# Performance work log

Measured on AMD Instinct MI355X. Metric: run time of the kernel, lower is better.

## Reference

```python
import jax, jax.numpy as jnp
import numpy as np
import math

EMBED_DIM = 512
NUM_HEADS = 8
HEAD_DIM = EMBED_DIM // NUM_HEADS


def setup_inputs() -> dict:
    key = jax.random.key(0)
    ks = jax.random.split(key, 11)
    s = 1.0 / math.sqrt(EMBED_DIM)
    x = jax.random.normal(ks[0], (8, EMBED_DIM, 32, 32), dtype=jnp.float32)
    Wq = jax.random.uniform(ks[1], (EMBED_DIM, EMBED_DIM), jnp.float32, -s, s)
    bq = jax.random.uniform(ks[2], (EMBED_DIM,), jnp.float32, -s, s)
    Wk = jax.random.uniform(ks[3], (EMBED_DIM, EMBED_DIM), jnp.float32, -s, s)
    bk = jax.random.uniform(ks[4], (EMBED_DIM,), jnp.float32, -s, s)
    Wv = jax.random.uniform(ks[5], (EMBED_DIM, EMBED_DIM), jnp.float32, -s, s)
    bv = jax.random.uniform(ks[6], (EMBED_DIM,), jnp.float32, -s, s)
    Wo = jax.random.uniform(ks[7], (EMBED_DIM, EMBED_DIM), jnp.float32, -s, s)
    bo = jax.random.uniform(ks[8], (EMBED_DIM,), jnp.float32, -s, s)
    gamma = jnp.ones((EMBED_DIM,), jnp.float32)
    beta = jnp.zeros((EMBED_DIM,), jnp.float32)
    return {"x": x, "Wq": Wq, "bq": bq, "Wk": Wk, "bk": bk, "Wv": Wv,
            "bv": bv, "Wo": Wo, "bo": bo, "gamma": gamma, "beta": beta}


def layer_norm(x, gamma, beta, eps=1e-5):
    mu = jnp.mean(x, axis=-1, keepdims=True)
    var = jnp.mean(jnp.square(x - mu), axis=-1, keepdims=True)
    return (x - mu) * jax.lax.rsqrt(var + eps) * gamma + beta


def reference(x, Wq, bq, Wk, bk, Wv, bv, Wo, bo, gamma, beta):
    B, C, H, W = x.shape
    S = H * W
    # [B, S, C]
    x_flat = x.reshape(B, C, S).transpose(0, 2, 1)
    residual = x_flat
    xn = layer_norm(x_flat, gamma, beta)
    # torch Linear: y = x @ W^T + b
    q = (xn @ Wq.T + bq).reshape(B, S, NUM_HEADS, HEAD_DIM)
    k = (xn @ Wk.T + bk).reshape(B, S, NUM_HEADS, HEAD_DIM)
    v = (xn @ Wv.T + bv).reshape(B, S, NUM_HEADS, HEAD_DIM)
    scale = 1.0 / math.sqrt(HEAD_DIM)
    scores = jnp.einsum('bqhd,bkhd->bhqk', q, k) * scale
    attn = jax.nn.softmax(scores, axis=-1)  # dropout is identity in eval
    out = jnp.einsum('bhqk,bkhd->bqhd', attn, v).reshape(B, S, C)
    out = out @ Wo.T + bo + residual
    return out.transpose(0, 2, 1).reshape(B, C, H, W)
```

## Files before the change

kernel.cpp:

```cpp
#include <hip/hip_runtime.h>
#include <hip/hip_bf16.h>

typedef __bf16 bf16_t;
typedef __bf16 bf16x8 __attribute__((ext_vector_type(8)));
typedef float floatx4 __attribute__((ext_vector_type(4)));

#define EMBED 512
#define S_LEN 1024
#define NH 8
#define HD 64
#define LDQ 1568

#define MFMA16(a, b, c) __builtin_amdgcn_mfma_f32_16x16x32_bf16(a, b, c, 0, 0, 0)

static __device__ __forceinline__ bf16_t f2bf(float f) {
    unsigned int x = __builtin_bit_cast(unsigned int, f);
    unsigned int lsb = (x >> 16) & 1u;
    x += 0x7fffu + lsb;
    unsigned short u = (unsigned short)(x >> 16);
    return __builtin_bit_cast(bf16_t, u);
}
static __device__ __forceinline__ float bf2f(bf16_t v) {
    unsigned short u = __builtin_bit_cast(unsigned short, v);
    unsigned int x = ((unsigned int)u) << 16;
    return __builtin_bit_cast(float, x);
}
static __device__ __forceinline__ unsigned int pack2(float lo, float hi) {
    return (__builtin_bit_cast(unsigned int, lo) >> 16) |
           (__builtin_bit_cast(unsigned int, hi) & 0xFFFF0000u);
}

__global__ __launch_bounds__(256) void cvt4_kernel(const float* __restrict__ s0,
                                                   const float* __restrict__ s1,
                                                   const float* __restrict__ s2,
                                                   const float* __restrict__ s3,
                                                   bf16_t* __restrict__ d0,
                                                   bf16_t* __restrict__ d1,
                                                   bf16_t* __restrict__ d2,
                                                   bf16_t* __restrict__ d3) {
    const float* s; bf16_t* d;
    switch (blockIdx.y) {
        case 0:  s = s0; d = d0; break;
        case 1:  s = s1; d = d1; break;
        case 2:  s = s2; d = d2; break;
        default: s = s3; d = d3; break;
    }
    int i = (blockIdx.x * 256 + threadIdx.x) * 8;
#pragma unroll
    for (int j = 0; j < 8; ++j) d[i + j] = f2bf(s[i + j]);
}

__global__ __launch_bounds__(256) void ln_stats_kernel(const float* __restrict__ x,
                                                       float* __restrict__ muA,
                                                       float* __restrict__ rsA) {
    int bid = blockIdx.x;
    int b = bid >> 5, s0 = (bid & 31) * 32;
    int t = threadIdx.x, tc = t >> 5, ts = t & 31;
    const float* xp = x + (size_t)b * EMBED * S_LEN + s0 + ts;
    float sm = 0.f, sq = 0.f;
    for (int i = 0; i < 64; ++i) {
        float v = xp[(size_t)(tc * 64 + i) * S_LEN];
        sm += v; sq += v * v;
    }
    __shared__ float Sm[8][32], Sq[8][32];
    Sm[tc][ts] = sm; Sq[tc][ts] = sq;
    __syncthreads();
    if (t < 32) {
        float m = 0.f, q = 0.f;
#pragma unroll
        for (int j = 0; j < 8; ++j) { m += Sm[j][t]; q += Sq[j][t]; }
        float mu = m * (1.0f / EMBED);
        float var = q * (1.0f / EMBED) - mu * mu;
        muA[b * S_LEN + s0 + t] = mu;
        rsA[b * S_LEN + s0 + t] = rsqrtf(var + 1e-5f);
    }
}

__global__ __launch_bounds__(256) void ln_tr_kernel(const float* __restrict__ x,
                                                    const float* __restrict__ muA,
                                                    const float* __restrict__ rsA,
                                                    const float* __restrict__ gamma,
                                                    const float* __restrict__ beta,
                                                    bf16_t* __restrict__ xn) {
    __shared__ float T[32][33];
    int tx = threadIdx.x & 31, ty = threadIdx.x >> 5;
    int b = blockIdx.z, c0 = blockIdx.y * 32, s0 = blockIdx.x * 32;
#pragma unroll
    for (int i = 0; i < 4; ++i) {
        int cr = ty + i * 8;
        T[cr][tx] = x[((size_t)b * EMBED + c0 + cr) * S_LEN + s0 + tx];
    }
    __syncthreads();
    float g = gamma[c0 + tx], be = beta[c0 + tx];
#pragma unroll
    for (int i = 0; i < 4; ++i) {
        int sr = ty + i * 8;
        float mu = muA[b * S_LEN + s0 + sr];
        float rs = rsA[b * S_LEN + s0 + sr];
        xn[((size_t)b * S_LEN + s0 + sr) * EMBED + c0 + tx] =
            f2bf((T[tx][sr] - mu) * rs * g + be);
    }
}

__global__ __launch_bounds__(256) void gemm_kernel(const bf16_t* __restrict__ X,
                                                   const bf16_t* __restrict__ W,
                                                   const float* __restrict__ b0,
                                                   const float* __restrict__ b1,
                                                   const float* __restrict__ b2,
                                                   bf16_t* __restrict__ Y, int ldY) {
    __shared__ __align__(16) bf16_t Wl[2][128 * 72];
    int t = threadIdx.x;
    int col0 = blockIdx.y * 128, row0 = blockIdx.x * 128;
    int scol = t >> 1, sseg = (t & 1) * 32;
    const bf16_t* wsrc = W + (size_t)(col0 + scol) * EMBED + sseg;
    {
        bf16x8 r0 = *(const bf16x8*)(wsrc);
        bf16x8 r1 = *(const bf16x8*)(wsrc + 8);
        bf16x8 r2 = *(const bf16x8*)(wsrc + 16);
        bf16x8 r3 = *(const bf16x8*)(wsrc + 24);
        bf16_t* d = &Wl[0][scol * 72 + sseg];
        *(bf16x8*)d = r0;        *(bf16x8*)(d + 8) = r1;
        *(bf16x8*)(d + 16) = r2; *(bf16x8*)(d + 24) = r3;
    }
    int lane = t & 63, w = t >> 6, g = lane >> 4, n16 = lane & 15;
    int rw0 = row0 + w * 32;
    const bf16_t* xr0 = X + (size_t)(rw0 + n16) * EMBED + g * 8;
    const bf16_t* xr1 = xr0 + (size_t)16 * EMBED;
    bf16x8 a00 = *(const bf16x8*)(xr0);
    bf16x8 a01 = *(const bf16x8*)(xr0 + 32);
    bf16x8 a10 = *(const bf16x8*)(xr1);
    bf16x8 a11 = *(const bf16x8*)(xr1 + 32);
    __syncthreads();
    floatx4 acc[2][8] = {};
#pragma unroll
    for (int kc = 0; kc < 8; ++kc) {
        bf16x8 p0, p1, p2, p3, na00, na01, na10, na11;
        if (kc < 7) {
            int ko = (kc + 1) * 64;
            p0 = *(const bf16x8*)(wsrc + ko);
            p1 = *(const bf16x8*)(wsrc + ko + 8);
            p2 = *(const bf16x8*)(wsrc + ko + 16);
            p3 = *(const bf16x8*)(wsrc + ko + 24);
            na00 = *(const bf16x8*)(xr0 + ko);
            na01 = *(const bf16x8*)(xr0 + ko + 32);
            na10 = *(const bf16x8*)(xr1 + ko);
            na11 = *(const bf16x8*)(xr1 + ko + 32);
        }
        const bf16_t* wl = &Wl[kc & 1][0];
#pragma unroll
        for (int kk = 0; kk < 2; ++kk) {
            bf16x8 s0 = (kk == 0) ? a00 : a01;
            bf16x8 s1 = (kk == 0) ? a10 : a11;
#pragma unroll
            for (int nt = 0; nt < 8; ++nt) {
                bf16x8 bfr = *(const bf16x8*)(&wl[(nt * 16 + n16) * 72 + kk * 32 + g * 8]);
                acc[0][nt] = MFMA16(s0, bfr, acc[0][nt]);
                acc[1][nt] = MFMA16(s1, bfr, acc[1][nt]);
            }
        }
        if (kc < 7) {
            bf16_t* d = &Wl[(kc + 1) & 1][scol * 72 + sseg];
            *(bf16x8*)d = p0;        *(bf16x8*)(d + 8) = p1;
            *(bf16x8*)(d + 16) = p2; *(bf16x8*)(d + 24) = p3;
            a00 = na00; a01 = na01; a10 = na10; a11 = na11;
        }
        __syncthreads();
    }
#pragma unroll
    for (int ar = 0; ar < 2; ++ar)
#pragma unroll
        for (int nt = 0; nt < 8; ++nt) {
            int col = col0 + nt * 16 + n16;
            float bv = (col < 512) ? b0[col]
                     : (col < 1024) ? b1[col - 512] : b2[col - 1024];
#pragma unroll
            for (int r = 0; r < 4; ++r) {
                int row = rw0 + ar * 16 + g * 4 + r;
                Y[(size_t)row * ldY + col] = f2bf(acc[ar][nt][r] + bv);
            }
        }
}

__global__ __launch_bounds__(256) void wsgemm_out_kernel(const bf16_t* __restrict__ Wb,
                                                         const bf16_t* __restrict__ act,
                                                         const float* __restrict__ bias,
                                                         const float* __restrict__ xres,
                                                         float* __restrict__ out) {
    __shared__ __align__(16) bf16_t Al[2][64 * 72];
    int b = blockIdx.z, n0 = blockIdx.x * 64, m0 = blockIdx.y * 128;
    int t = threadIdx.x;
    int srow = t >> 2, sseg = (t & 3) * 16;
    const bf16_t* asrc = act + ((size_t)b * S_LEN + n0 + srow) * EMBED + sseg;
    {
        bf16x8 r0 = *(const bf16x8*)(asrc);
        bf16x8 r1 = *(const bf16x8*)(asrc + 8);
        bf16_t* d = &Al[0][srow * 72 + sseg];
        *(bf16x8*)d = r0; *(bf16x8*)(d + 8) = r1;
    }
    int lane = t & 63, w = t >> 6, g = lane >> 4, n16 = lane & 15;
    int mw = m0 + w * 32;
    const bf16_t* wr0 = Wb + (size_t)(mw + n16) * EMBED + g * 8;
    const bf16_t* wr1 = wr0 + (size_t)16 * EMBED;
    bf16x8 a00 = *(const bf16x8*)(wr0);
    bf16x8 a01 = *(const bf16x8*)(wr0 + 32);
    bf16x8 a10 = *(const bf16x8*)(wr1);
    bf16x8 a11 = *(const bf16x8*)(wr1 + 32);
    __syncthreads();
    floatx4 acc[2][4] = {};
#pragma unroll
    for (int kc = 0; kc < 8; ++kc) {
        bf16x8 p0, p1, na00, na01, na10, na11;
        if (kc < 7) {
            int ko = (kc + 1) * 64;
            p0 = *(const bf16x8*)(asrc + ko);
            p1 = *(const bf16x8*)(asrc + ko + 8);
            na00 = *(const bf16x8*)(wr0 + ko);
            na01 = *(const bf16x8*)(wr0 + ko + 32);
            na10 = *(const bf16x8*)(wr1 + ko);
            na11 = *(const bf16x8*)(wr1 + ko + 32);
        }
        const bf16_t* al = &Al[kc & 1][0];
#pragma unroll
        for (int kk = 0; kk < 2; ++kk) {
            bf16x8 s0 = (kk == 0) ? a00 : a01;
            bf16x8 s1 = (kk == 0) ? a10 : a11;
#pragma unroll
            for (int nt = 0; nt < 4; ++nt) {
                bf16x8 bfr = *(const bf16x8*)(&al[(nt * 16 + n16) * 72 + kk * 32 + g * 8]);
                acc[0][nt] = MFMA16(s0, bfr, acc[0][nt]);
                acc[1][nt] = MFMA16(s1, bfr, acc[1][nt]);
            }
        }
        if (kc < 7) {
            bf16_t* d = &Al[(kc + 1) & 1][srow * 72 + sseg];
            *(bf16x8*)d = p0; *(bf16x8*)(d + 8) = p1;
            a00 = na00; a01 = na01; a10 = na10; a11 = na11;
        }
        __syncthreads();
    }
#pragma unroll
    for (int ar = 0; ar < 2; ++ar)
#pragma unroll
        for (int r = 0; r < 4; ++r) {
            int row = mw + ar * 16 + g * 4 + r;
            float bv = bias[row];
#pragma unroll
            for (int nt = 0; nt < 4; ++nt) {
                int col = n0 + nt * 16 + n16;
                size_t oi = ((size_t)b * EMBED + row) * S_LEN + col;
                out[oi] = acc[ar][nt][r] + bv + xres[oi];
            }
        }
}

__global__ __launch_bounds__(256) void attn_kernel(const bf16_t* __restrict__ qkv,
                                                   bf16_t* __restrict__ o) {
    __shared__ __align__(16) bf16_t Kt[2][64 * 72];
    __shared__ __align__(16) bf16_t Vt[2][64 * 72];
    __shared__ __align__(16) unsigned int Pl[4][2][16 * 36];
    int bid = blockIdx.x;
    int bh = bid & 63, qt = bid >> 6;
    int b = bh >> 3, h = bh & 7;
    int t = threadIdx.x, w = t >> 6, lane = t & 63, g = lane >> 4, n16 = lane & 15;
    size_t baseQ = (size_t)b * S_LEN * LDQ + h * HD;
    int qA = qt * 128 + w * 32 + n16;

    const bf16_t* qpA = qkv + baseQ + (size_t)qA * LDQ + g * 8;
    const bf16_t* qpB = qpA + (size_t)16 * LDQ;
    bf16x8 qa0 = *(const bf16x8*)(qpA);
    bf16x8 qa1 = *(const bf16x8*)(qpA + 32);
    bf16x8 qb0 = *(const bf16x8*)(qpB);
    bf16x8 qb1 = *(const bf16x8*)(qpB + 32);
#pragma unroll
    for (int j = 0; j < 8; ++j) {
        qa0[j] = f2bf(bf2f(qa0[j]) * 0.125f);
        qa1[j] = f2bf(bf2f(qa1[j]) * 0.125f);
        qb0[j] = f2bf(bf2f(qb0[j]) * 0.125f);
        qb1[j] = f2bf(bf2f(qb1[j]) * 0.125f);
    }

    int srow = t >> 2, scol = (t & 3) * 16;
    const bf16_t* ksrc = qkv + baseQ + 512 + (size_t)srow * LDQ + scol;
    const bf16_t* vsrc = qkv + baseQ + 1024 + (size_t)srow * LDQ + scol;
    {
        bf16x8 k0 = *(const bf16x8*)(ksrc);
        bf16x8 k1 = *(const bf16x8*)(ksrc + 8);
        bf16x8 v0 = *(const bf16x8*)(vsrc);
        bf16x8 v1 = *(const bf16x8*)(vsrc + 8);
        bf16_t* kd = &Kt[0][srow * 72 + scol];
        *(bf16x8*)kd = k0; *(bf16x8*)(kd + 8) = k1;
#pragma unroll
        for (int j = 0; j < 8; ++j) {
            Vt[0][(scol + j) * 72 + srow]     = v0[j];
            Vt[0][(scol + 8 + j) * 72 + srow] = v1[j];
        }
    }

    float lsA[4] = {}, lsB[4] = {};
    floatx4 oaccA[4] = {}, oaccB[4] = {};
    unsigned int* PLa = &Pl[w][0][0];
    unsigned int* PLb = &Pl[w][1][0];

    for (int it = 0; it < 16; ++it) {
        int cur = it & 1, nxt = cur ^ 1;
        __syncthreads();
        bf16x8 pk0, pk1, pv0, pv1;
        if (it < 15) {
            size_t adv = (size_t)(it + 1) * 64 * LDQ;
            pk0 = *(const bf16x8*)(ksrc + adv);
            pk1 = *(const bf16x8*)(ksrc + adv + 8);
            pv0 = *(const bf16x8*)(vsrc + adv);
            pv1 = *(const bf16x8*)(vsrc + adv + 8);
        }
        const bf16_t* Kl = &Kt[cur][0];
        const bf16_t* Vl = &Vt[cur][0];
        floatx4 sA[4], sB[4];
#pragma unroll
        for (int kb = 0; kb < 4; ++kb) {
            bf16x8 k0 = *(const bf16x8*)(&Kl[(kb * 16 + n16) * 72 + g * 8]);
            bf16x8 k1 = *(const bf16x8*)(&Kl[(kb * 16 + n16) * 72 + 32 + g * 8]);
            sA[kb] = floatx4{-12.f, -12.f, -12.f, -12.f};
            sA[kb] = MFMA16(k0, qa0, sA[kb]);
            sA[kb] = MFMA16(k1, qa1, sA[kb]);
            sB[kb] = floatx4{-12.f, -12.f, -12.f, -12.f};
            sB[kb] = MFMA16(k0, qb0, sB[kb]);
            sB[kb] = MFMA16(k1, qb1, sB[kb]);
        }
        if (it < 15) {
            bf16_t* kd = &Kt[nxt][srow * 72 + scol];
            *(bf16x8*)kd = pk0; *(bf16x8*)(kd + 8) = pk1;
#pragma unroll
            for (int j = 0; j < 8; ++j) {
                Vt[nxt][(scol + j) * 72 + srow]     = pv0[j];
                Vt[nxt][(scol + 8 + j) * 72 + srow] = pv1[j];
            }
        }
#pragma unroll
        for (int kb = 0; kb < 4; ++kb)
#pragma unroll
            for (int r = 0; r < 4; ++r) {
                float eA = __expf(fminf(sA[kb][r], 40.f));
                sA[kb][r] = eA; lsA[kb] += eA;
                float eB = __expf(fminf(sB[kb][r], 40.f));
                sB[kb][r] = eB; lsB[kb] += eB;
            }
#pragma unroll
        for (int kb = 0; kb < 4; ++kb) {
            uint2 prA, prB;
            prA.x = pack2(sA[kb][0], sA[kb][1]);
            prA.y = pack2(sA[kb][2], sA[kb][3]);
            *(uint2*)&PLa[n16 * 36 + kb * 8 + g * 2] = prA;
            prB.x = pack2(sB[kb][0], sB[kb][1]);
            prB.y = pack2(sB[kb][2], sB[kb][3]);
            *(uint2*)&PLb[n16 * 36 + kb * 8 + g * 2] = prB;
        }
        uint4 uA0 = *(const uint4*)&PLa[n16 * 36 + g * 4];
        uint4 uA1 = *(const uint4*)&PLa[n16 * 36 + 16 + g * 4];
        uint4 uB0 = *(const uint4*)&PLb[n16 * 36 + g * 4];
        uint4 uB1 = *(const uint4*)&PLb[n16 * 36 + 16 + g * 4];
        bf16x8 pfA0 = __builtin_bit_cast(bf16x8, uA0);
        bf16x8 pfA1 = __builtin_bit_cast(bf16x8, uA1);
        bf16x8 pfB0 = __builtin_bit_cast(bf16x8, uB0);
        bf16x8 pfB1 = __builtin_bit_cast(bf16x8, uB1);
#pragma unroll
        for (int dt = 0; dt < 4; ++dt) {
            bf16x8 v0 = *(const bf16x8*)(&Vl[(dt * 16 + n16) * 72 + g * 8]);
            bf16x8 v1 = *(const bf16x8*)(&Vl[(dt * 16 + n16) * 72 + 32 + g * 8]);
            oaccA[dt] = MFMA16(v0, pfA0, oaccA[dt]);
            oaccA[dt] = MFMA16(v1, pfA1, oaccA[dt]);
            oaccB[dt] = MFMA16(v0, pfB0, oaccB[dt]);
            oaccB[dt] = MFMA16(v1, pfB1, oaccB[dt]);
        }
    }
    float lA = (lsA[0] + lsA[1]) + (lsA[2] + lsA[3]);
    lA += __shfl_xor(lA, 16);
    lA += __shfl_xor(lA, 32);
    float lB = (lsB[0] + lsB[1]) + (lsB[2] + lsB[3]);
    lB += __shfl_xor(lB, 16);
    lB += __shfl_xor(lB, 32);
    float rlA = 1.0f / lA, rlB = 1.0f / lB;
    size_t orowA = ((size_t)b * S_LEN + qA) * EMBED + h * HD;
    size_t orowB = orowA + (size_t)16 * EMBED;
#pragma unroll
    for (int dt = 0; dt < 4; ++dt) {
        uint2 prA, prB;
        prA.x = pack2(oaccA[dt][0] * rlA, oaccA[dt][1] * rlA);
        prA.y = pack2(oaccA[dt][2] * rlA, oaccA[dt][3] * rlA);
        *(uint2*)(o + orowA + dt * 16 + g * 4) = prA;
        prB.x = pack2(oaccB[dt][0] * rlB, oaccB[dt][1] * rlB);
        prB.y = pack2(oaccB[dt][2] * rlB, oaccB[dt][3] * rlB);
        *(uint2*)(o + orowB + dt * 16 + g * 4) = prB;
    }
}

extern "C" void kernel_launch(void* const* d_in, const int* in_sizes, int n_in,
                              void* d_out, int out_size, void* d_ws, size_t ws_size,
                              hipStream_t stream) {
    const float* x     = (const float*)d_in[0];
    const float* Wq    = (const float*)d_in[1];
    const float* bq    = (const float*)d_in[2];
    const float* Wk    = (const float*)d_in[3];
    const float* bk    = (const float*)d_in[4];
    const float* Wv    = (const float*)d_in[5];
    const float* bv    = (const float*)d_in[6];
    const float* Wo    = (const float*)d_in[7];
    const float* bo    = (const float*)d_in[8];
    const float* gamma = (const float*)d_in[9];
    const float* beta  = (const float*)d_in[10];
    float* out = (float*)d_out;

    char* ws = (char*)d_ws;
    bf16_t* xn    = (bf16_t*)ws;
    bf16_t* qkvb  = (bf16_t*)(ws + 8388608);
    bf16_t* wqkv  = (bf16_t*)(ws + 34078720);
    bf16_t* wo    = (bf16_t*)(ws + 35651584);
    float*  muA   = (float*)(ws + 36175872);
    float*  rsA   = (float*)(ws + 36208640);
    bf16_t* ab    = xn;

    cvt4_kernel<<<dim3(128, 4), 256, 0, stream>>>(Wq, Wk, Wv, Wo,
                                                  wqkv, wqkv + 262144,
                                                  wqkv + 524288, wo);
    ln_stats_kernel<<<dim3(256), 256, 0, stream>>>(x, muA, rsA);
    ln_tr_kernel<<<dim3(32, 16, 8), 256, 0, stream>>>(x, muA, rsA, gamma, beta, xn);
    gemm_kernel<<<dim3(64, 12), 256, 0, stream>>>(xn, wqkv, bq, bk, bv, qkvb, LDQ);
    attn_kernel<<<dim3(512), 256, 0, stream>>>(qkvb, ab);
    wsgemm_out_kernel<<<dim3(16, 4, 8), 256, 0, stream>>>(wo, ab, bo, x, out);
}
```

Baseline: 180.1 us.

## Emit V transposed from QKV GEMM epilogue to drop per-tile LDS transpose in attention

The QKV projection now writes Q/K into a narrower row-major buffer and writes V in a per-channel (transposed) layout via an LDS-staged epilogue, storing it temporarily in the output buffer. The attention kernel then loads V tiles with vectorized contiguous reads and 16-byte LDS stores instead of 16 scalar scattered LDS writes per thread per tile. This targets LDS bank conflicts and scalar-store overhead in the attention inner loop, at the cost of an extra barrier and LDS round-trip in the GEMM epilogue and reuse of the output buffer as scratch.

```diff
diff --git a/kernel.cpp b/kernel.cpp
--- a/kernel.cpp
+++ b/kernel.cpp
@@ -9,7 +9,8 @@
 #define S_LEN 1024
 #define NH 8
 #define HD 64
-#define LDQ 1568
+#define LDK 1056
+#define LDV 1088
 
 #define MFMA16(a, b, c) __builtin_amdgcn_mfma_f32_16x16x32_bf16(a, b, c, 0, 0, 0)
 
@@ -28,6 +29,11 @@
 static __device__ __forceinline__ unsigned int pack2(float lo, float hi) {
     return (__builtin_bit_cast(unsigned int, lo) >> 16) |
            (__builtin_bit_cast(unsigned int, hi) & 0xFFFF0000u);
+}
+static __device__ __forceinline__ unsigned int pack2r(float lo, float hi) {
+    unsigned short a = __builtin_bit_cast(unsigned short, f2bf(lo));
+    unsigned short b = __builtin_bit_cast(unsigned short, f2bf(hi));
+    return (unsigned int)a | ((unsigned int)b << 16);
 }
 
 __global__ __launch_bounds__(256) void cvt4_kernel(const float* __restrict__ s0,
@@ -107,7 +113,8 @@
                                                    const float* __restrict__ b0,
                                                    const float* __restrict__ b1,
                                                    const float* __restrict__ b2,
-                                                   bf16_t* __restrict__ Y, int ldY) {
+                                                   bf16_t* __restrict__ Y,
+                                                   bf16_t* __restrict__ vtb) {
     __shared__ __align__(16) bf16_t Wl[2][128 * 72];
     int t = threadIdx.x;
     int col0 = blockIdx.y * 128, row0 = blockIdx.x * 128;
@@ -166,19 +173,42 @@
         }
         __syncthreads();
     }
-#pragma unroll
-    for (int ar = 0; ar < 2; ++ar)
-#pragma unroll
-        for (int nt = 0; nt < 8; ++nt) {
-            int col = col0 + nt * 16 + n16;
-            float bv = (col < 512) ? b0[col]
-                     : (col < 1024) ? b1[col - 512] : b2[col - 1024];
-#pragma unroll
-            for (int r = 0; r < 4; ++r) {
-                int row = rw0 + ar * 16 + g * 4 + r;
-                Y[(size_t)row * ldY + col] = f2bf(acc[ar][nt][r] + bv);
-            }
-        }
+    if (col0 < 1024) {
+        const float* bp = (col0 < 512) ? b0 : b1;
+#pragma unroll
+        for (int ar = 0; ar < 2; ++ar)
+#pragma unroll
+            for (int nt = 0; nt < 8; ++nt) {
+                int col = col0 + nt * 16 + n16;
+                float bv = bp[col & 511];
+#pragma unroll
+                for (int r = 0; r < 4; ++r) {
+                    int row = rw0 + ar * 16 + g * 4 + r;
+                    Y[(size_t)row * LDK + col] = f2bf(acc[ar][nt][r] + bv);
+                }
+            }
+    } else {
+        bf16_t* Tl = &Wl[0][0];
+#pragma unroll
+        for (int ar = 0; ar < 2; ++ar)
+#pragma unroll
+            for (int nt = 0; nt < 8; ++nt) {
+                int chl = nt * 16 + n16;
+                float bv = b2[(col0 & 511) + chl];
+                uint2 pr;
+                pr.x = pack2r(acc[ar][nt][0] + bv, acc[ar][nt][1] + bv);
+                pr.y = pack2r(acc[ar][nt][2] + bv, acc[ar][nt][3] + bv);
+                *(uint2*)(&Tl[chl * 136 + w * 32 + ar * 16 + g * 4]) = pr;
+            }
+        __syncthreads();
+        int ch = t >> 1, seg = (t & 1) * 64;
+        int bb = row0 >> 10, s0 = row0 & 1023;
+        bf16_t* dst = vtb + ((size_t)(bb * EMBED + (col0 - 1024) + ch)) * LDV + s0 + seg;
+        const bf16_t* srcl = &Tl[ch * 136 + seg];
+#pragma unroll
+        for (int i = 0; i < 8; ++i)
+            *(bf16x8*)(dst + i * 8) = *(const bf16x8*)(srcl + i * 8);
+    }
 }
 
 __global__ __launch_bounds__(256) void wsgemm_out_kernel(const bf16_t* __restrict__ Wb,
@@ -253,20 +283,22 @@
         }
 }
 
-__global__ __launch_bounds__(256) void attn_kernel(const bf16_t* __restrict__ qkv,
+__global__ __launch_bounds__(256) void attn_kernel(const bf16_t* __restrict__ qk,
+                                                   const bf16_t* __restrict__ vt,
                                                    bf16_t* __restrict__ o) {
     __shared__ __align__(16) bf16_t Kt[2][64 * 72];
-    __shared__ __align__(16) bf16_t Vt[2][64 * 72];
+    __shared__ __align__(16) bf16_t Vl2[2][64 * 72];
     __shared__ __align__(16) unsigned int Pl[4][2][16 * 36];
     int bid = blockIdx.x;
     int bh = bid & 63, qt = bid >> 6;
     int b = bh >> 3, h = bh & 7;
     int t = threadIdx.x, w = t >> 6, lane = t & 63, g = lane >> 4, n16 = lane & 15;
-    size_t baseQ = (size_t)b * S_LEN * LDQ + h * HD;
+    size_t baseQK = (size_t)b * S_LEN * LDK;
+    size_t baseV  = ((size_t)b * EMBED + h * HD) * LDV;
     int qA = qt * 128 + w * 32 + n16;
 
-    const bf16_t* qpA = qkv + baseQ + (size_t)qA * LDQ + g * 8;
-    const bf16_t* qpB = qpA + (size_t)16 * LDQ;
+    const bf16_t* qpA = qk + baseQK + (size_t)qA * LDK + h * HD + g * 8;
+    const bf16_t* qpB = qpA + (size_t)16 * LDK;
     bf16x8 qa0 = *(const bf16x8*)(qpA);
     bf16x8 qa1 = *(const bf16x8*)(qpA + 32);
     bf16x8 qb0 = *(const bf16x8*)(qpB);
@@ -278,22 +310,21 @@
         qb0[j] = f2bf(bf2f(qb0[j]) * 0.125f);
         qb1[j] = f2bf(bf2f(qb1[j]) * 0.125f);
     }
+    const bf16_t* kbase = qk + baseQK + 512 + h * HD;
+    const bf16_t* vbase = vt + baseV;
 
     int srow = t >> 2, scol = (t & 3) * 16;
-    const bf16_t* ksrc = qkv + baseQ + 512 + (size_t)srow * LDQ + scol;
-    const bf16_t* vsrc = qkv + baseQ + 1024 + (size_t)srow * LDQ + scol;
+    const bf16_t* ksrc = kbase + (size_t)srow * LDK + scol;
+    const bf16_t* vsrc = vbase + (size_t)srow * LDV + scol;
     {
         bf16x8 k0 = *(const bf16x8*)(ksrc);
         bf16x8 k1 = *(const bf16x8*)(ksrc + 8);
         bf16x8 v0 = *(const bf16x8*)(vsrc);
         bf16x8 v1 = *(const bf16x8*)(vsrc + 8);
         bf16_t* kd = &Kt[0][srow * 72 + scol];
+        bf16_t* vd = &Vl2[0][srow * 72 + scol];
         *(bf16x8*)kd = k0; *(bf16x8*)(kd + 8) = k1;
-#pragma unroll
-        for (int j = 0; j < 8; ++j) {
-            Vt[0][(scol + j) * 72 + srow]     = v0[j];
-            Vt[0][(scol + 8 + j) * 72 + srow] = v1[j];
-        }
+        *(bf16x8*)vd = v0; *(bf16x8*)(vd + 8) = v1;
     }
 
     float lsA[4] = {}, lsB[4] = {};
@@ -306,14 +337,15 @@
         __syncthreads();
         bf16x8 pk0, pk1, pv0, pv1;
         if (it < 15) {
-            size_t adv = (size_t)(it + 1) * 64 * LDQ;
-            pk0 = *(const bf16x8*)(ksrc + adv);
-            pk1 = *(const bf16x8*)(ksrc + adv + 8);
-            pv0 = *(const bf16x8*)(vsrc + adv);
-            pv1 = *(const bf16x8*)(vsrc + adv + 8);
+            const bf16_t* kp = ksrc + (size_t)(it + 1) * 64 * LDK;
+            pk0 = *(const bf16x8*)(kp);
+            pk1 = *(const bf16x8*)(kp + 8);
+            const bf16_t* vp = vsrc + (it + 1) * 64;
+            pv0 = *(const bf16x8*)(vp);
+            pv1 = *(const bf16x8*)(vp + 8);
         }
         const bf16_t* Kl = &Kt[cur][0];
-        const bf16_t* Vl = &Vt[cur][0];
+        const bf16_t* Vl = &Vl2[cur][0];
         floatx4 sA[4], sB[4];
 #pragma unroll
         for (int kb = 0; kb < 4; ++kb) {
@@ -328,12 +360,9 @@
         }
         if (it < 15) {
             bf16_t* kd = &Kt[nxt][srow * 72 + scol];
+            bf16_t* vd = &Vl2[nxt][srow * 72 + scol];
             *(bf16x8*)kd = pk0; *(bf16x8*)(kd + 8) = pk1;
-#pragma unroll
-            for (int j = 0; j < 8; ++j) {
-                Vt[nxt][(scol + j) * 72 + srow]     = pv0[j];
-                Vt[nxt][(scol + 8 + j) * 72 + srow] = pv1[j];
-            }
+            *(bf16x8*)vd = pv0; *(bf16x8*)(vd + 8) = pv1;
         }
 #pragma unroll
         for (int kb = 0; kb < 4; ++kb)
@@ -411,19 +440,21 @@
 
     char* ws = (char*)d_ws;
     bf16_t* xn    = (bf16_t*)ws;
-    bf16_t* qkvb  = (bf16_t*)(ws + 8388608);
-    bf16_t* wqkv  = (bf16_t*)(ws + 34078720);
-    bf16_t* wo    = (bf16_t*)(ws + 35651584);
-    float*  muA   = (float*)(ws + 36175872);
-    float*  rsA   = (float*)(ws + 36208640);
+    bf16_t* qkb   = (bf16_t*)(ws + 8388608);
+    bf16_t* wqkv  = (bf16_t*)(ws + 25690112);
+    bf16_t* wo    = (bf16_t*)(ws + 27262976);
+    float*  muA   = (float*)(ws + 27787264);
+    float*  rsA   = (float*)(ws + 27820032);
     bf16_t* ab    = xn;
+
+    bf16_t* vtb = (bf16_t*)d_out;
 
     cvt4_kernel<<<dim3(128, 4), 256, 0, stream>>>(Wq, Wk, Wv, Wo,
                                                   wqkv, wqkv + 262144,
                                                   wqkv + 524288, wo);
     ln_stats_kernel<<<dim3(256), 256, 0, stream>>>(x, muA, rsA);
     ln_tr_kernel<<<dim3(32, 16, 8), 256, 0, stream>>>(x, muA, rsA, gamma, beta, xn);
-    gemm_kernel<<<dim3(64, 12), 256, 0, stream>>>(xn, wqkv, bq, bk, bv, qkvb, LDQ);
-    attn_kernel<<<dim3(512), 256, 0, stream>>>(qkvb, ab);
+    gemm_kernel<<<dim3(64, 12), 256, 0, stream>>>(xn, wqkv, bq, bk, bv, qkb, vtb);
+    attn_kernel<<<dim3(512), 256, 0, stream>>>(qkb, vtb, ab);
     wsgemm_out_kernel<<<dim3(16, 4, 8), 256, 0, stream>>>(wo, ab, bo, x, out);
 }
```

Result: faster. 171.1 us (-5.0%).
